# Kernel tuning notes

Measured on AMD Instinct MI355X. Metric: run time of the kernel, lower is better.

## Reference

```python
import jax, jax.numpy as jnp
import numpy as np
from jax import lax

THRESHOLDS = (0.25, 0.5, 0.75)
TAU = 100.0
NUM_CLASSES = 10
K = 32
RES_Z = 5.0
# each of the 16 binary logic gates is bilinear: g(a,b) = c0 + c1*a + c2*b + c3*a*b
GATE_COEF = jnp.array([
    [0, 0, 0, 0],   # 0: False
    [0, 0, 0, 1],   # 1: a AND b
    [0, 1, 0, -1],  # 2: a AND NOT b
    [0, 1, 0, 0],   # 3: a  (residual gate)
    [0, 0, 1, -1],  # 4: NOT a AND b
    [0, 0, 1, 0],   # 5: b
    [0, 1, 1, -2],  # 6: XOR
    [0, 1, 1, -1],  # 7: OR
    [1, -1, -1, 1], # 8: NOR
    [1, -1, -1, 2], # 9: XNOR
    [1, 0, -1, 0],  # 10: NOT b
    [1, 0, -1, 1],  # 11: a OR NOT b
    [1, -1, 0, 0],  # 12: NOT a
    [1, -1, 0, 1],  # 13: NOT a OR b
    [1, 0, 0, -1],  # 14: NAND
    [1, 0, 0, 0],   # 15: True
], dtype=jnp.float32)


def _gate_logits(key, shape):
    # residual init: pass-through gate (id 3) dominates
    w = 0.01 * jax.random.normal(key, shape, dtype=jnp.float32)
    return w.at[..., 3].add(RES_Z)


def _leaf_idx(rng, C, O, leaves=8, cpt=2, kk=9):
    # each tree uses cpt random input channels; each leaf picks one of them and a 3x3 position
    ch2 = rng.integers(0, C, size=(O, cpt))
    sel = rng.integers(0, cpt, size=(O, leaves))
    ch = np.take_along_axis(ch2, sel, axis=1)
    pos = rng.integers(0, kk, size=(O, leaves))
    return jnp.asarray(ch * kk + pos, dtype=jnp.int32)


def setup_inputs() -> dict:
    key = jax.random.key(0)
    ks = jax.random.split(key, 9)
    rng = np.random.default_rng(0)
    B = 128
    d = {"x": jax.random.uniform(ks[0], (B, 3, 32, 32), dtype=jnp.float32)}
    in_chs = [3 * len(THRESHOLDS), K, 4 * K, 16 * K]
    out_chs = [K, 4 * K, 16 * K, 32 * K]
    for i, (ci, co) in enumerate(zip(in_chs, out_chs)):
        d[f"c{i+1}_idx"] = _leaf_idx(rng, ci, co)
        d[f"c{i+1}_w"] = _gate_logits(ks[1 + i], (co, 7, 16))
    dims = [32 * K * 4, 1280 * K, 640 * K, 320 * K]
    for i in range(3):
        di, do = dims[i], dims[i + 1]
        d[f"l{i+1}_a"] = jnp.asarray(rng.integers(0, di, size=(do,)), dtype=jnp.int32)
        d[f"l{i+1}_b"] = jnp.asarray(rng.integers(0, di, size=(do,)), dtype=jnp.int32)
        d[f"l{i+1}_w"] = _gate_logits(ks[5 + i], (do, 16))
    return d


def _mix(logits):
    # softmax over 16 gates folded into 4 bilinear coefficients (fused gate mixture)
    return jax.nn.softmax(logits, axis=-1) @ GATE_COEF


def binarize(x):
    return jnp.concatenate([(x > t).astype(x.dtype) for t in THRESHOLDS], axis=1)


def tree_conv(x, leaf_idx, logits):
    # x: (B,C,H,W); leaf_idx: (O,8) into C*9 channel-major patch; logits: (O,7,16)
    B, C, H, W = x.shape
    xp = jnp.pad(x, ((0, 0), (0, 0), (1, 1), (1, 1)))
    patches = jnp.stack([xp[:, :, i:i + H, j:j + W] for i in range(3) for j in range(3)], axis=2)
    patches = patches.reshape(B, C * 9, H, W)
    vals = patches[:, leaf_idx]  # (B,O,8,H,W)
    m = _mix(logits)             # (O,7,4)
    node = 0
    for lvl in (4, 2, 1):
        a, b = vals[:, :, 0::2], vals[:, :, 1::2]
        w = m[:, node:node + lvl]  # (O,lvl,4)
        w0 = w[..., 0][None, :, :, None, None]
        w1 = w[..., 1][None, :, :, None, None]
        w2 = w[..., 2][None, :, :, None, None]
        w3 = w[..., 3][None, :, :, None, None]
        vals = w0 + w1 * a + w2 * b + w3 * (a * b)
        node += lvl
    return vals[:, :, 0]  # (B,O,H,W)


def or_pool(x):
    # OR of relaxed binary values == max pool 2x2/2
    return lax.reduce_window(x, -jnp.inf, lax.max, (1, 1, 2, 2), (1, 1, 2, 2), "VALID")


def logic_layer(x, a_idx, b_idx, logits):
    a = x[:, a_idx]  # (B,O)
    b = x[:, b_idx]
    w = _mix(logits)  # (O,4)
    return w[:, 0] + w[:, 1] * a + w[:, 2] * b + w[:, 3] * (a * b)


def group_sum(x):
    B = x.shape[0]
    return x.reshape(B, NUM_CLASSES, -1).sum(axis=-1) / TAU


def reference(x, c1_idx, c1_w, c2_idx, c2_w, c3_idx, c3_w, c4_idx, c4_w,
              l1_a, l1_b, l1_w, l2_a, l2_b, l2_w, l3_a, l3_b, l3_w):
    h = binarize(x)
    h = or_pool(tree_conv(h, c1_idx, c1_w))
    h = or_pool(tree_conv(h, c2_idx, c2_w))
    h = or_pool(tree_conv(h, c3_idx, c3_w))
    h = or_pool(tree_conv(h, c4_idx, c4_w))
    h = h.reshape(h.shape[0], -1)  # (B, 4096)
    h = logic_layer(h, l1_a, l1_b, l1_w)
    h = logic_layer(h, l2_a, l2_b, l2_w)
    h = logic_layer(h, l3_a, l3_b, l3_w)
    return group_sum(h)  # (B, 10)
```

## Files before the change

### kernel.cpp

```cpp
#include <hip/hip_runtime.h>

#define BATCH 128

typedef float v2f __attribute__((ext_vector_type(2)));
typedef float v4f __attribute__((ext_vector_type(4)));

__device__ __constant__ float GC[16][4] = {
  {0,0,0,0},{0,0,0,1},{0,1,0,-1},{0,1,0,0},
  {0,0,1,-1},{0,0,1,0},{0,1,1,-2},{0,1,1,-1},
  {1,-1,-1,1},{1,-1,-1,2},{1,0,-1,0},{1,0,-1,1},
  {1,-1,0,0},{1,-1,0,1},{1,0,0,-1},{1,0,0,0}};

__device__ __forceinline__ v2f pk_mul(v2f a, v2f b) {
  v2f d;
  asm("v_pk_mul_f32 %0, %1, %2" : "=v"(d) : "v"(a), "v"(b));
  return d;
}
__device__ __forceinline__ v2f max2(v2f a, v2f b) {
  v2f d;
  d.x = fmaxf(a.x, b.x);
  d.y = fmaxf(a.y, b.y);
  return d;
}
__device__ __forceinline__ v2f gate2pk(v2f a, v2f b, v2f w01, v2f w23) {
  v2f t = pk_mul(a, b);
  v2f d;
  asm("v_pk_fma_f32 %0, %1, %2, %2 op_sel:[0,1,0] op_sel_hi:[1,1,0]"
      : "=v"(d) : "v"(a), "v"(w01));
  asm("v_pk_fma_f32 %0, %1, %2, %0 op_sel:[0,0,0] op_sel_hi:[1,0,1]"
      : "+v"(d) : "v"(b), "v"(w23));
  asm("v_pk_fma_f32 %0, %1, %2, %0 op_sel:[0,1,0] op_sel_hi:[1,1,1]"
      : "+v"(d) : "v"(t), "v"(w23));
  return d;
}

__device__ __forceinline__ void mix_one(const float* lp, float* op) {
  float e[16];
  float s = 0.f;
  #pragma unroll
  for (int i = 0; i < 16; ++i) { e[i] = __expf(lp[i]); s += e[i]; }
  float inv = 1.0f / s;
  float w0 = 0.f, w1 = 0.f, w2 = 0.f, w3 = 0.f;
  #pragma unroll
  for (int i = 0; i < 16; ++i) {
    float p = e[i] * inv;
    w0 = fmaf(p, GC[i][0], w0);
    w1 = fmaf(p, GC[i][1], w1);
    w2 = fmaf(p, GC[i][2], w2);
    w3 = fmaf(p, GC[i][3], w3);
  }
  op[0] = w0; op[1] = w1; op[2] = w2; op[3] = w3;
}

struct PrepArgs {
  const float* x;
  const float* logits[7];
  float* outm[7];
  float* xtb;
  float* out;
};

__global__ __launch_bounds__(256) void prep_k(PrepArgs A) {
  __shared__ float tile[64 * 129];
  int blk = blockIdx.x;
  if (blk < 327) {
    int gid = blk * 256 + threadIdx.x;
    const int n[7] = {224, 896, 3584, 7168, 40960, 20480, 10240};
    if (gid < 83552) {
      int g = gid, seg = 0;
      while (seg < 6 && g >= n[seg]) { g -= n[seg]; ++seg; }
      mix_one(A.logits[seg] + (size_t)g * 16, A.outm[seg] + (size_t)g * 4);
    }
  } else if (blk < 327 + 144) {
    int tb = blk - 327;
    int c    = tb / 16;
    int pix0 = (tb % 16) * 64;
    int ti = c / 3, rgb = c - ti * 3;
    float th = 0.25f * (float)(ti + 1);
    {
      int pix = threadIdx.x & 63;
      int b0  = threadIdx.x >> 6;
      #pragma unroll 4
      for (int i = 0; i < 32; ++i) {
        int b = b0 + i * 4;
        float xv = A.x[(size_t)(b * 3 + rgb) * 1024 + pix0 + pix];
        tile[pix * 129 + b] = (xv > th) ? 1.f : 0.f;
      }
    }
    __syncthreads();
    {
      int b  = threadIdx.x & 127;
      int p0 = threadIdx.x >> 7;
      #pragma unroll 4
      for (int i = 0; i < 32; ++i) {
        int pix = p0 + i * 2;
        A.xtb[(size_t)(c * 1024 + pix0 + pix) * BATCH + b] = tile[pix * 129 + b];
      }
    }
  } else {
    int t = threadIdx.x;
    #pragma unroll
    for (int i = 0; i < 5; ++i) A.out[t * 5 + i] = 0.f;
  }
}

template <int H, int W>
__global__ __launch_bounds__(256) void conv_t(
    const float* __restrict__ in_t, const int* __restrict__ li_g,
    const float* __restrict__ m, float* __restrict__ out_t) {
  constexpr int PH = H / 2, PWD = W / 2, PIX = PH * PWD;
  int wave = threadIdx.x >> 6;
  int b2   = threadIdx.x & 63;
  int q = __builtin_amdgcn_readfirstlane(blockIdx.x * 4 + wave);
  int o = q / PIX;
  int p = q - o * PIX;
  int ph = p / PWD;
  int pw = p - ph * PWD;

  const int* li = li_g + o * 8;
  const v4f* mv = (const v4f*)(m + o * 28);
  v4f g0 = mv[0], g1 = mv[1], g2 = mv[2], g3 = mv[3];
  v4f g4 = mv[4], g5 = mv[5], g6 = mv[6];

  v2f best = {-1e30f, -1e30f};
  #pragma unroll
  for (int half = 0; half < 2; ++half) {
    v2f v[2][8];
    #pragma unroll
    for (int l = 0; l < 8; ++l) {
      int idx = li[l];
      int c = idx / 9;
      int k = idx - c * 9;
      int di = k / 3 - 1;
      int dj = (k - (k / 3) * 3) - 1;
      const float* base = in_t + (size_t)(c * H * W) * BATCH;
      int y = 2 * ph + half + di;
      #pragma unroll
      for (int pi = 0; pi < 2; ++pi) {
        int x = 2 * pw + pi + dj;
        v2f val = {0.f, 0.f};
        if ((unsigned)y < (unsigned)H && (unsigned)x < (unsigned)W)
          val = ((const v2f*)(base + (size_t)(y * W + x) * BATCH))[b2];
        v[pi][l] = val;
      }
    }
    #pragma unroll
    for (int pi = 0; pi < 2; ++pi) {
      v2f u0 = gate2pk(v[pi][0], v[pi][1], g0.xy, g0.zw);
      v2f u1 = gate2pk(v[pi][2], v[pi][3], g1.xy, g1.zw);
      v2f u2 = gate2pk(v[pi][4], v[pi][5], g2.xy, g2.zw);
      v2f u3 = gate2pk(v[pi][6], v[pi][7], g3.xy, g3.zw);
      v2f s0 = gate2pk(u0, u1, g4.xy, g4.zw);
      v2f s1 = gate2pk(u2, u3, g5.xy, g5.zw);
      v2f r  = gate2pk(s0, s1, g6.xy, g6.zw);
      best = max2(best, r);
    }
  }
  ((v2f*)(out_t + (size_t)q * BATCH))[b2] = best;
}

__global__ __launch_bounds__(256) void logic_k(
    const float* __restrict__ in, const int* __restrict__ aidx,
    const int* __restrict__ bidx, const float* __restrict__ m,
    float* __restrict__ out) {
  int wave = threadIdx.x >> 6;
  int b2   = threadIdx.x & 63;
  int j0 = blockIdx.x * 16 + wave;
  #pragma unroll
  for (int it = 0; it < 4; ++it) {
    int j = __builtin_amdgcn_readfirstlane(j0 + it * 4);
    int ai = aidx[j];
    int bi = bidx[j];
    v4f w = ((const v4f*)m)[j];
    v2f a = ((const v2f*)(in + (size_t)ai * BATCH))[b2];
    v2f b = ((const v2f*)(in + (size_t)bi * BATCH))[b2];
    ((v2f*)(out + (size_t)j * BATCH))[b2] = gate2pk(a, b, w.xy, w.zw);
  }
}

__global__ __launch_bounds__(256) void logic3_gsum_k(
    const float* __restrict__ in, const int* __restrict__ aidx,
    const int* __restrict__ bidx, const float* __restrict__ m,
    float* __restrict__ out) {
  __shared__ v2f red[4][64];
  int wave = threadIdx.x >> 6;
  int b2   = threadIdx.x & 63;
  int base = __builtin_amdgcn_readfirstlane(blockIdx.x * 256 + wave * 64);
  int cls  = base >> 10;
  v2f s = {0.f, 0.f};
  #pragma unroll 4
  for (int it = 0; it < 64; ++it) {
    int j = base + it;
    int ai = aidx[j];
    int bi = bidx[j];
    v4f w = ((const v4f*)m)[j];
    v2f a = ((const v2f*)(in + (size_t)ai * BATCH))[b2];
    v2f b = ((const v2f*)(in + (size_t)bi * BATCH))[b2];
    s += gate2pk(a, b, w.xy, w.zw);
  }
  red[wave][b2] = s;
  __syncthreads();
  if (threadIdx.x < 64) {
    v2f t = red[0][b2] + red[1][b2] + red[2][b2] + red[3][b2];
    atomicAdd(&out[(2 * b2) * 10 + cls], t.x * 0.01f);
    atomicAdd(&out[(2 * b2 + 1) * 10 + cls], t.y * 0.01f);
  }
}

extern "C" void kernel_launch(void* const* d_in, const int* in_sizes, int n_in,
                              void* d_out, int out_size, void* d_ws, size_t ws_size,
                              hipStream_t stream) {
  const float* x   = (const float*)d_in[0];
  const int*   c1i = (const int*)d_in[1];
  const float* c1w = (const float*)d_in[2];
  const int*   c2i = (const int*)d_in[3];
  const float* c2w = (const float*)d_in[4];
  const int*   c3i = (const int*)d_in[5];
  const float* c3w = (const float*)d_in[6];
  const int*   c4i = (const int*)d_in[7];
  const float* c4w = (const float*)d_in[8];
  const int*   l1a = (const int*)d_in[9];
  const int*   l1b = (const int*)d_in[10];
  const float* l1w = (const float*)d_in[11];
  const int*   l2a = (const int*)d_in[12];
  const int*   l2b = (const int*)d_in[13];
  const float* l2w = (const float*)d_in[14];
  const int*   l3a = (const int*)d_in[15];
  const int*   l3b = (const int*)d_in[16];
  const float* l3w = (const float*)d_in[17];

  float* ws = (float*)d_ws;
  float* mc1 = ws;
  float* mc2 = mc1 + 896;
  float* mc3 = mc2 + 3584;
  float* mc4 = mc3 + 14336;
  float* ml1 = mc4 + 28672;
  float* ml2 = ml1 + 163840;
  float* ml3 = ml2 + 81920;
  float* xtb = ml3 + 40960;
  float* h1  = xtb + 1179648;
  float* h2  = h1 + 1048576;
  float* h3  = h2 + 1048576;
  float* h4  = h3 + 1048576;
  float* g1  = h4 + 524288;
  float* g2  = g1 + 5242880;

  PrepArgs A;
  A.x = x;
  A.logits[0] = c1w; A.outm[0] = mc1;
  A.logits[1] = c2w; A.outm[1] = mc2;
  A.logits[2] = c3w; A.outm[2] = mc3;
  A.logits[3] = c4w; A.outm[3] = mc4;
  A.logits[4] = l1w; A.outm[4] = ml1;
  A.logits[5] = l2w; A.outm[5] = ml2;
  A.logits[6] = l3w; A.outm[6] = ml3;
  A.xtb = xtb;
  A.out = (float*)d_out;
  prep_k<<<472, 256, 0, stream>>>(A);

  conv_t<32, 32><<<8192 / 4, 256, 0, stream>>>(xtb, c1i, mc1, h1);
  conv_t<16, 16><<<8192 / 4, 256, 0, stream>>>(h1, c2i, mc2, h2);
  conv_t<8, 8><<<8192 / 4, 256, 0, stream>>>(h2, c3i, mc3, h3);
  conv_t<4, 4><<<4096 / 4, 256, 0, stream>>>(h3, c4i, mc4, h4);

  logic_k<<<40960 / 16, 256, 0, stream>>>(h4, l1a, l1b, ml1, g1);
  logic_k<<<20480 / 16, 256, 0, stream>>>(g1, l2a, l2b, ml2, g2);
  logic3_gsum_k<<<40, 256, 0, stream>>>(g2, l3a, l3b, ml3, (float*)d_out);
}
```

Before: 157.7 us.

## Fuse three logic layers into one kernel recomputing upstream gates per output

Replaces the separate logic-layer kernels with a single kernel where each final-layer output recomputes its four first-layer and two second-layer gates directly from the conv output. This removes the large intermediate g1/g2 global writes and reads and two launches, at the cost of redundant gather and gate work. The atomic group sum is replaced by per-block partial sums and a small final reduction kernel, so output zeroing in prep is dropped.

Measured after the change: 161.1 us. +2.1%, slower.

```diff
diff --git a/kernel.cpp b/kernel.cpp
--- a/kernel.cpp
+++ b/kernel.cpp
@@ -57,7 +57,6 @@
   const float* logits[7];
   float* outm[7];
   float* xtb;
-  float* out;
 };
 
 __global__ __launch_bounds__(256) void prep_k(PrepArgs A) {
@@ -71,7 +70,7 @@
       while (seg < 6 && g >= n[seg]) { g -= n[seg]; ++seg; }
       mix_one(A.logits[seg] + (size_t)g * 16, A.outm[seg] + (size_t)g * 4);
     }
-  } else if (blk < 327 + 144) {
+  } else {
     int tb = blk - 327;
     int c    = tb / 16;
     int pix0 = (tb % 16) * 64;
@@ -97,10 +96,6 @@
         A.xtb[(size_t)(c * 1024 + pix0 + pix) * BATCH + b] = tile[pix * 129 + b];
       }
     }
-  } else {
-    int t = threadIdx.x;
-    #pragma unroll
-    for (int i = 0; i < 5; ++i) A.out[t * 5 + i] = 0.f;
   }
 }
 
@@ -159,52 +154,71 @@
   ((v2f*)(out_t + (size_t)q * BATCH))[b2] = best;
 }
 
-__global__ __launch_bounds__(256) void logic_k(
-    const float* __restrict__ in, const int* __restrict__ aidx,
-    const int* __restrict__ bidx, const float* __restrict__ m,
-    float* __restrict__ out) {
-  int wave = threadIdx.x >> 6;
-  int b2   = threadIdx.x & 63;
-  int j0 = blockIdx.x * 16 + wave;
-  #pragma unroll
-  for (int it = 0; it < 4; ++it) {
-    int j = __builtin_amdgcn_readfirstlane(j0 + it * 4);
-    int ai = aidx[j];
-    int bi = bidx[j];
-    v4f w = ((const v4f*)m)[j];
-    v2f a = ((const v2f*)(in + (size_t)ai * BATCH))[b2];
-    v2f b = ((const v2f*)(in + (size_t)bi * BATCH))[b2];
-    ((v2f*)(out + (size_t)j * BATCH))[b2] = gate2pk(a, b, w.xy, w.zw);
-  }
-}
-
-__global__ __launch_bounds__(256) void logic3_gsum_k(
-    const float* __restrict__ in, const int* __restrict__ aidx,
-    const int* __restrict__ bidx, const float* __restrict__ m,
-    float* __restrict__ out) {
+struct LFArgs {
+  const float* h4;
+  const int *l1a, *l1b, *l2a, *l2b, *l3a, *l3b;
+  const float *ml1, *ml2, *ml3;
+  float* part;
+};
+
+__global__ __launch_bounds__(256) void logic_fused_k(LFArgs A) {
   __shared__ v2f red[4][64];
   int wave = threadIdx.x >> 6;
   int b2   = threadIdx.x & 63;
-  int base = __builtin_amdgcn_readfirstlane(blockIdx.x * 256 + wave * 64);
-  int cls  = base >> 10;
+  int base = __builtin_amdgcn_readfirstlane(blockIdx.x * 32 + wave * 8);
+
   v2f s = {0.f, 0.f};
-  #pragma unroll 4
-  for (int it = 0; it < 64; ++it) {
-    int j = base + it;
-    int ai = aidx[j];
-    int bi = bidx[j];
-    v4f w = ((const v4f*)m)[j];
-    v2f a = ((const v2f*)(in + (size_t)ai * BATCH))[b2];
-    v2f b = ((const v2f*)(in + (size_t)bi * BATCH))[b2];
-    s += gate2pk(a, b, w.xy, w.zw);
+  #pragma unroll
+  for (int it = 0; it < 8; ++it) {
+    int j  = base + it;
+    int a3 = A.l3a[j];
+    int b3 = A.l3b[j];
+    int xa = A.l2a[a3], xb = A.l2b[a3];
+    int ya = A.l2a[b3], yb = A.l2b[b3];
+
+    v4f wxa = ((const v4f*)A.ml1)[xa];
+    v4f wxb = ((const v4f*)A.ml1)[xb];
+    v4f wya = ((const v4f*)A.ml1)[ya];
+    v4f wyb = ((const v4f*)A.ml1)[yb];
+    v4f wa  = ((const v4f*)A.ml2)[a3];
+    v4f wb  = ((const v4f*)A.ml2)[b3];
+    v4f wj  = ((const v4f*)A.ml3)[j];
+
+    const float* h4 = A.h4;
+    v2f hxa0 = ((const v2f*)(h4 + (size_t)A.l1a[xa] * BATCH))[b2];
+    v2f hxa1 = ((const v2f*)(h4 + (size_t)A.l1b[xa] * BATCH))[b2];
+    v2f hxb0 = ((const v2f*)(h4 + (size_t)A.l1a[xb] * BATCH))[b2];
+    v2f hxb1 = ((const v2f*)(h4 + (size_t)A.l1b[xb] * BATCH))[b2];
+    v2f hya0 = ((const v2f*)(h4 + (size_t)A.l1a[ya] * BATCH))[b2];
+    v2f hya1 = ((const v2f*)(h4 + (size_t)A.l1b[ya] * BATCH))[b2];
+    v2f hyb0 = ((const v2f*)(h4 + (size_t)A.l1a[yb] * BATCH))[b2];
+    v2f hyb1 = ((const v2f*)(h4 + (size_t)A.l1b[yb] * BATCH))[b2];
+
+    v2f g1xa = gate2pk(hxa0, hxa1, wxa.xy, wxa.zw);
+    v2f g1xb = gate2pk(hxb0, hxb1, wxb.xy, wxb.zw);
+    v2f g1ya = gate2pk(hya0, hya1, wya.xy, wya.zw);
+    v2f g1yb = gate2pk(hyb0, hyb1, wyb.xy, wyb.zw);
+    v2f g2a  = gate2pk(g1xa, g1xb, wa.xy, wa.zw);
+    v2f g2b  = gate2pk(g1ya, g1yb, wb.xy, wb.zw);
+    s += gate2pk(g2a, g2b, wj.xy, wj.zw);
   }
   red[wave][b2] = s;
   __syncthreads();
   if (threadIdx.x < 64) {
     v2f t = red[0][b2] + red[1][b2] + red[2][b2] + red[3][b2];
-    atomicAdd(&out[(2 * b2) * 10 + cls], t.x * 0.01f);
-    atomicAdd(&out[(2 * b2 + 1) * 10 + cls], t.y * 0.01f);
-  }
+    ((v2f*)(A.part + (size_t)blockIdx.x * BATCH))[b2] = t;
+  }
+}
+
+__global__ __launch_bounds__(128) void gsum_final_k(
+    const float* __restrict__ part, float* __restrict__ out) {
+  int cls = blockIdx.x;
+  int b   = threadIdx.x;
+  const float* p = part + (size_t)cls * 32 * BATCH + b;
+  float s = 0.f;
+  #pragma unroll
+  for (int k = 0; k < 32; ++k) s += p[(size_t)k * BATCH];
+  out[b * 10 + cls] = s * 0.01f;
 }
 
 extern "C" void kernel_launch(void* const* d_in, const int* in_sizes, int n_in,
@@ -242,8 +256,7 @@
   float* h2  = h1 + 1048576;
   float* h3  = h2 + 1048576;
   float* h4  = h3 + 1048576;
-  float* g1  = h4 + 524288;
-  float* g2  = g1 + 5242880;
+  float* part = h4 + 524288;
 
   PrepArgs A;
   A.x = x;
@@ -255,15 +268,21 @@
   A.logits[5] = l2w; A.outm[5] = ml2;
   A.logits[6] = l3w; A.outm[6] = ml3;
   A.xtb = xtb;
-  A.out = (float*)d_out;
-  prep_k<<<472, 256, 0, stream>>>(A);
+  prep_k<<<471, 256, 0, stream>>>(A);
 
   conv_t<32, 32><<<8192 / 4, 256, 0, stream>>>(xtb, c1i, mc1, h1);
   conv_t<16, 16><<<8192 / 4, 256, 0, stream>>>(h1, c2i, mc2, h2);
   conv_t<8, 8><<<8192 / 4, 256, 0, stream>>>(h2, c3i, mc3, h3);
   conv_t<4, 4><<<4096 / 4, 256, 0, stream>>>(h3, c4i, mc4, h4);
 
-  logic_k<<<40960 / 16, 256, 0, stream>>>(h4, l1a, l1b, ml1, g1);
-  logic_k<<<20480 / 16, 256, 0, stream>>>(g1, l2a, l2b, ml2, g2);
-  logic3_gsum_k<<<40, 256, 0, stream>>>(g2, l3a, l3b, ml3, (float*)d_out);
-}
+  LFArgs L;
+  L.h4 = h4;
+  L.l1a = l1a; L.l1b = l1b;
+  L.l2a = l2a; L.l2b = l2b;
+  L.l3a = l3a; L.l3b = l3b;
+  L.ml1 = ml1; L.ml2 = ml2; L.ml3 = ml3;
+  L.part = part;
+  logic_fused_k<<<320, 256, 0, stream>>>(L);
+
+  gsum_final_k<<<10, 128, 0, stream>>>(part, (float*)d_out);
+}
```

## Load both horizontal pool pixels per leaf with one 16-byte load in tree conv

Applied to the files above, without the earlier changes.

Each lane in the tree-conv kernel now loads a float4 that covers two adjacent pixels for four batch elements, instead of two separate float2 loads per leaf. The upper half-wave handles the second pixel of the 2x2 pool window. A cross-half shuffle then takes the max of the two pixels and the lower 32 lanes write the result. This halves the number of load instructions and keeps them contiguous. The cost is extra shuffles, edge-case branches and half-idle stores.

Result: slower. 161.3 us (+2.3%).

```diff
diff --git a/kernel.cpp b/kernel.cpp
--- a/kernel.cpp
+++ b/kernel.cpp
@@ -14,12 +14,6 @@
 __device__ __forceinline__ v2f pk_mul(v2f a, v2f b) {
   v2f d;
   asm("v_pk_mul_f32 %0, %1, %2" : "=v"(d) : "v"(a), "v"(b));
-  return d;
-}
-__device__ __forceinline__ v2f max2(v2f a, v2f b) {
-  v2f d;
-  d.x = fmaxf(a.x, b.x);
-  d.y = fmaxf(a.y, b.y);
   return d;
 }
 __device__ __forceinline__ v2f gate2pk(v2f a, v2f b, v2f w01, v2f w23) {
@@ -31,6 +25,18 @@
       : "+v"(d) : "v"(b), "v"(w23));
   asm("v_pk_fma_f32 %0, %1, %2, %0 op_sel:[0,1,0] op_sel_hi:[1,1,1]"
       : "+v"(d) : "v"(t), "v"(w23));
+  return d;
+}
+__device__ __forceinline__ v4f gate4pk(v4f a, v4f b, v2f w01, v2f w23) {
+  v4f r;
+  r.xy = gate2pk(a.xy, b.xy, w01, w23);
+  r.zw = gate2pk(a.zw, b.zw, w01, w23);
+  return r;
+}
+__device__ __forceinline__ v4f max4(v4f a, v4f b) {
+  v4f d;
+  d.x = fmaxf(a.x, b.x); d.y = fmaxf(a.y, b.y);
+  d.z = fmaxf(a.z, b.z); d.w = fmaxf(a.w, b.w);
   return d;
 }
 
@@ -110,7 +116,8 @@
     const float* __restrict__ m, float* __restrict__ out_t) {
   constexpr int PH = H / 2, PWD = W / 2, PIX = PH * PWD;
   int wave = threadIdx.x >> 6;
-  int b2   = threadIdx.x & 63;
+  int lane = threadIdx.x & 63;
+  int xi   = lane >> 5;
   int q = __builtin_amdgcn_readfirstlane(blockIdx.x * 4 + wave);
   int o = q / PIX;
   int p = q - o * PIX;
@@ -122,10 +129,10 @@
   v4f g0 = mv[0], g1 = mv[1], g2 = mv[2], g3 = mv[3];
   v4f g4 = mv[4], g5 = mv[5], g6 = mv[6];
 
-  v2f best = {-1e30f, -1e30f};
+  v4f best = {-1e30f, -1e30f, -1e30f, -1e30f};
   #pragma unroll
   for (int half = 0; half < 2; ++half) {
-    v2f v[2][8];
+    v4f v[8];
     #pragma unroll
     for (int l = 0; l < 8; ++l) {
       int idx = li[l];
@@ -133,30 +140,42 @@
       int k = idx - c * 9;
       int di = k / 3 - 1;
       int dj = (k - (k / 3) * 3) - 1;
-      const float* base = in_t + (size_t)(c * H * W) * BATCH;
-      int y = 2 * ph + half + di;
-      #pragma unroll
-      for (int pi = 0; pi < 2; ++pi) {
-        int x = 2 * pw + pi + dj;
-        v2f val = {0.f, 0.f};
-        if ((unsigned)y < (unsigned)H && (unsigned)x < (unsigned)W)
-          val = ((const v2f*)(base + (size_t)(y * W + x) * BATCH))[b2];
-        v[pi][l] = val;
+      const float* plane = in_t + (size_t)(c * H * W) * BATCH;
+      int y  = 2 * ph + half + di;
+      int xb = 2 * pw + dj;
+      v4f val = {0.f, 0.f, 0.f, 0.f};
+      if ((unsigned)y < (unsigned)H) {
+        bool vlo = (xb >= 0);
+        bool vhi = (xb + 1 < W);
+        int px0 = y * W + xb;
+        if (vlo && vhi) {
+          val = ((const v4f*)(plane + (size_t)px0 * BATCH))[lane];
+        } else {
+          int pv = vlo ? px0 : (px0 + 1);
+          v4f t = ((const v4f*)(plane + (size_t)pv * BATCH))[lane & 31];
+          v4f z = {0.f, 0.f, 0.f, 0.f};
+          val = (xi == (vlo ? 0 : 1)) ? t : z;
+        }
       }
-    }
-    #pragma unroll
-    for (int pi = 0; pi < 2; ++pi) {
-      v2f u0 = gate2pk(v[pi][0], v[pi][1], g0.xy, g0.zw);
-      v2f u1 = gate2pk(v[pi][2], v[pi][3], g1.xy, g1.zw);
-      v2f u2 = gate2pk(v[pi][4], v[pi][5], g2.xy, g2.zw);
-      v2f u3 = gate2pk(v[pi][6], v[pi][7], g3.xy, g3.zw);
-      v2f s0 = gate2pk(u0, u1, g4.xy, g4.zw);
-      v2f s1 = gate2pk(u2, u3, g5.xy, g5.zw);
-      v2f r  = gate2pk(s0, s1, g6.xy, g6.zw);
-      best = max2(best, r);
-    }
-  }
-  ((v2f*)(out_t + (size_t)q * BATCH))[b2] = best;
+      v[l] = val;
+    }
+    v4f u0 = gate4pk(v[0], v[1], g0.xy, g0.zw);
+    v4f u1 = gate4pk(v[2], v[3], g1.xy, g1.zw);
+    v4f u2 = gate4pk(v[4], v[5], g2.xy, g2.zw);
+    v4f u3 = gate4pk(v[6], v[7], g3.xy, g3.zw);
+    v4f s0 = gate4pk(u0, u1, g4.xy, g4.zw);
+    v4f s1 = gate4pk(u2, u3, g5.xy, g5.zw);
+    v4f r  = gate4pk(s0, s1, g6.xy, g6.zw);
+    best = max4(best, r);
+  }
+  v4f other;
+  other.x = __shfl_xor(best.x, 32, 64);
+  other.y = __shfl_xor(best.y, 32, 64);
+  other.z = __shfl_xor(best.z, 32, 64);
+  other.w = __shfl_xor(best.w, 32, 64);
+  best = max4(best, other);
+  if (lane < 32)
+    ((v4f*)(out_t + (size_t)q * BATCH))[lane] = best;
 }
 
 __global__ __launch_bounds__(256) void logic_k(
```
